# Performance work log

Measured on AMD Instinct MI355X. Metric: run time of the kernel, lower is better.

## Reference

```python
import jax, jax.numpy as jnp
import numpy as np

DIM = 384
NUM_HEADS = 12
WIN = (8, 8, 8)
Q_TOK = 1
K_TOK = 1
B = 64
N = WIN[0] * WIN[1] * WIN[2]  # 512


def _build_rel_index():
    t = max(Q_TOK, K_TOK)
    max_rel = [(w - 1) * t for w in WIN]
    nbins = [2 * m + 1 for m in max_rel]
    def coords(tok):
        axes = [np.arange(WIN[i]) * tok for i in range(3)]
        g = np.stack(np.meshgrid(*axes, indexing='ij'))  # [3, D, H, W]
        return g.reshape(3, -1)  # [3, N]
    cq = coords(Q_TOK)
    ck = coords(K_TOK)
    rel = (cq[:, :, None] - ck[:, None, :]).transpose(1, 2, 0)  # [N, N, 3]
    rel = rel + np.array(max_rel)
    idx = rel[..., 0] * (nbins[1] * nbins[2]) + rel[..., 1] * nbins[2] + rel[..., 2]
    return idx.astype(np.int32), nbins[0] * nbins[1] * nbins[2]


def setup_inputs() -> dict:
    key = jax.random.key(0)
    ks = jax.random.split(key, 7)
    rel_index_np, num_rel = _build_rel_index()
    s = 0.02
    return {
        'x1': jax.random.normal(ks[0], (B, N, DIM), jnp.float32),
        'x2': jax.random.normal(ks[1], (B, N, DIM), jnp.float32),
        'Wq': jax.random.normal(ks[2], (DIM, DIM), jnp.float32) * s,
        'Wkv': jax.random.normal(ks[3], (2 * DIM, DIM), jnp.float32) * s,
        'q_bias': jax.random.normal(ks[4], (DIM,), jnp.float32) * s,
        'v_bias': jax.random.normal(ks[5], (DIM,), jnp.float32) * s,
        'bias_table': jax.random.normal(ks[6], (num_rel, NUM_HEADS), jnp.float32) * s,
        'rel_index': jnp.asarray(rel_index_np),  # [N, N] int32
    }


def reference(x1, x2, Wq, Wkv, q_bias, v_bias, bias_table, rel_index):
    Bq, N1, C = x1.shape
    N2 = x2.shape[1]
    H = NUM_HEADS
    hd = C // H

    q = x1 @ Wq.T + q_bias                      # [B, N1, C]
    kv_bias = jnp.concatenate([jnp.zeros_like(v_bias), v_bias])
    kv = x2 @ Wkv.T + kv_bias                   # [B, N2, 2C]

    q = q.reshape(Bq, N1, H, hd).transpose(0, 2, 1, 3)   # [B, H, N1, hd]
    kv = kv.reshape(Bq, N2, 2, H, hd).transpose(2, 0, 3, 1, 4)
    k, v = kv[0], kv[1]                          # [B, H, N2, hd]

    # relative position bias: gather [N1, N2, H] -> [H, N1, N2]
    bias = bias_table[rel_index]                 # [N1, N2, H]
    bias = bias.transpose(2, 0, 1)               # [H, N1, N2]

    scale = 1.0 / jnp.sqrt(jnp.asarray(hd, q.dtype))
    scores = jnp.einsum('bhqd,bhkd->bhqk', q, k) * scale + bias[None]
    attn = jax.nn.softmax(scores, axis=-1)
    out = jnp.einsum('bhqk,bhkd->bhqd', attn, v)  # [B, H, N1, hd]
    return out.transpose(0, 2, 1, 3).reshape(Bq, N1, C)
```

## Files before the change

### kernel.cpp

```cpp
#include <hip/hip_runtime.h>

typedef unsigned short u16;
typedef unsigned int u32;
typedef __bf16 bf16x8 __attribute__((ext_vector_type(8)));
typedef float f32x4 __attribute__((ext_vector_type(4)));
typedef u16 u16x8 __attribute__((ext_vector_type(8)));
typedef u32 u32x4 __attribute__((ext_vector_type(4)));

#define NB 64
#define NN 512
#define NH 12
#define HD 32
#define DIM 384

static constexpr size_t QWS = (size_t)NB * NH * NN * HD;
#define LOG2E 1.4426950408889634f
#define QSCALE 0.25503486f

__device__ __forceinline__ u16 f2bf(float f) {
  __bf16 b = (__bf16)f;
  union { __bf16 b; u16 u; } v; v.b = b;
  return v.u;
}
__device__ __forceinline__ float lo16f(u32 w) {
  union { u32 u; float f; } v; v.u = w << 16;
  return v.f;
}
__device__ __forceinline__ float hi16f(u32 w) {
  union { u32 u; float f; } v; v.u = w & 0xffff0000u;
  return v.f;
}
__device__ __forceinline__ void gload16(const void* g, void* l) {
  __builtin_amdgcn_global_load_lds((const __attribute__((address_space(1))) u32*)g,
                                   (__attribute__((address_space(3))) u32*)l, 16, 0, 0);
}

__global__ __launch_bounds__(256) void prep_k(const float* __restrict__ table,
                                              const int* __restrict__ rel,
                                              const float* __restrict__ Wq,
                                              const float* __restrict__ Wkv,
                                              u32* __restrict__ beR,
                                              u16* __restrict__ Wf) {
  int bid = blockIdx.x;
  if (bid < 6144) {
    int t = bid * 256 + threadIdx.x;
    int word = t & 3;
    int lane = (t >> 2) & 63;
    int mf   = (t >> 8) & 3;
    int wv   = (t >> 10) & 7;
    int kt   = (t >> 13) & 15;
    int h    = t >> 17;
    int lr = lane & 15, lg = lane >> 4;
    int q = wv * 64 + mf * 16 + lr;
    int k = kt * 32 + (word >> 1) * 16 + lg * 4 + (word & 1) * 2;
    int i0 = rel[q * NN + k];
    int i1 = rel[q * NN + k + 1];
    u16 b0 = f2bf(table[i0 * NH + h] * LOG2E);
    u16 b1 = f2bf(table[i1 * NH + h] * LOG2E);
    beR[t] = (u32)b0 | ((u32)b1 << 16);
  } else {
    int t2 = (bid - 6144) * 256 + threadIdx.x;
    int lane = t2 & 63;
    int kk = (t2 >> 6) % 12;
    int cb = t2 / (12 * 64);
    int j = cb * 16 + (lane & 15);
    int k = kk * 32 + (lane >> 4) * 8;
    const float* wrow = (j < 384) ? (Wq + (size_t)j * DIM) : (Wkv + (size_t)(j - 384) * DIM);
    float4 a = *(const float4*)(wrow + k);
    float4 b = *(const float4*)(wrow + k + 4);
    u16x8 o = {f2bf(a.x), f2bf(a.y), f2bf(a.z), f2bf(a.w),
               f2bf(b.x), f2bf(b.y), f2bf(b.z), f2bf(b.w)};
    *(u16x8*)(Wf + (size_t)t2 * 8) = o;
  }
}

__global__ __launch_bounds__(512, 4) void qkv_proj_k(const float* __restrict__ x1,
                                                     const float* __restrict__ x2,
                                                     const float* __restrict__ qb,
                                                     const float* __restrict__ vb,
                                                     const u16* __restrict__ Wf,
                                                     u16* __restrict__ q_ws,
                                                     u16* __restrict__ k_ws,
                                                     u16* __restrict__ v_ws) {
  __shared__ __attribute__((aligned(16))) u16 Wbuf[2][12288];

  const int bid = blockIdx.x;
  const int is_q = bid >= 256;
  const int m0 = (bid & 255) * 128;
  const int tid = threadIdx.x, lane = tid & 63, w = tid >> 6;
  const int lg = lane >> 4, lr = lane & 15;
  const float* X = is_q ? x1 : x2;
  const int cb0 = is_q ? 0 : 24;
  const int nch = is_q ? 12 : 24;
  const char* wsrc = (const char*)(Wf + (size_t)cb0 * 12 * 64 * 8);
  const int bb = m0 >> 9;

  bf16x8 af[12];
  const float* xrow = X + (size_t)(m0 + w * 16 + lr) * DIM + lg * 8;
#pragma unroll
  for (int kk = 0; kk < 12; ++kk) {
    float4 a = *(const float4*)(xrow + kk * 32);
    float4 b = *(const float4*)(xrow + kk * 32 + 4);
    af[kk] = (bf16x8){(__bf16)a.x, (__bf16)a.y, (__bf16)a.z, (__bf16)a.w,
                      (__bf16)b.x, (__bf16)b.y, (__bf16)b.z, (__bf16)b.w};
  }

#pragma unroll
  for (int i = 0; i < 3; ++i) {
    int inst = w + i * 8;
    gload16(wsrc + inst * 1024 + lane * 16, (char*)&Wbuf[0][0] + inst * 1024 + lane * 16);
  }
  __syncthreads();

  for (int c = 0; c < nch; ++c) {
    if (c + 1 < nch) {
      const char* s = wsrc + (size_t)(c + 1) * 24576;
      char* d = (char*)&Wbuf[(c + 1) & 1][0];
#pragma unroll
      for (int i = 0; i < 3; ++i) {
        int inst = w + i * 8;
        gload16(s + inst * 1024 + lane * 16, d + inst * 1024 + lane * 16);
      }
    }
    const u16* wb = &Wbuf[c & 1][0];
#pragma unroll
    for (int lc = 0; lc < 2; ++lc) {
      f32x4 acc = {0.f, 0.f, 0.f, 0.f};
#pragma unroll
      for (int kk = 0; kk < 12; ++kk) {
        bf16x8 wf = *(const bf16x8*)(wb + ((lc * 12 + kk) * 64 + lane) * 8);
        acc = __builtin_amdgcn_mfma_f32_16x16x32_bf16(af[kk], wf, acc, 0, 0, 0);
      }
      int j = (cb0 + c * 2 + lc) * 16 + lr;
      int jj = is_q ? j : (j < 768 ? j - 384 : j - 768);
      float bv = is_q ? qb[jj] : (j >= 768 ? vb[jj] : 0.0f);
      float scale = is_q ? QSCALE : 1.0f;
      u16* dst = is_q ? q_ws : (j < 768 ? k_ws : v_ws);
      int hh = jj >> 5, dd = jj & 31;
      size_t basead = ((size_t)(bb * NH + hh) * NN) * HD + dd;
      int rowb = (m0 & 511) + w * 16 + lg * 4;
#pragma unroll
      for (int r = 0; r < 4; ++r)
        dst[basead + (size_t)(rowb + r) * HD] = f2bf((acc[r] + bv) * scale);
    }
    __syncthreads();
  }
}

__global__ __launch_bounds__(512, 4) void attn_k(const u16* __restrict__ qw,
                                                 const u16* __restrict__ kw,
                                                 const u16* __restrict__ vw,
                                                 const u32* __restrict__ beR,
                                                 float* __restrict__ out) {
  const int g = blockIdx.x;
  const int vv = (g & 7) * 96 + (g >> 3);
  const int h = vv >> 6, b = vv & 63;
  const size_t base = ((size_t)b * NH + h) * NN * HD;
  const u16* Q = qw + base;
  const u16* K = kw + base;
  const u16* V = vw + base;

  __shared__ u16 Ks[NN][40];
  __shared__ u16 Vtp[HD][520];

  const int tid = threadIdx.x;
  const int lane = tid & 63, w = tid >> 6;
  const int lg = lane >> 4, lr = lane & 15;
  const int q0 = w * 64;

  bf16x8 qf[4];
#pragma unroll
  for (int mf = 0; mf < 4; ++mf)
    qf[mf] = *(const bf16x8*)&Q[(q0 + mf * 16 + lr) * HD + lg * 8];

  for (int c = tid; c < 2048; c += 512) {
    int row = c >> 2, part = (c & 3) * 8;
    *(u16x8*)&Ks[row][part] = *(const u16x8*)&K[row * HD + part];
    u16x8 vld = *(const u16x8*)&V[row * HD + part];
    int kk = row & 31;
    int col = (row & ~31) + ((kk >> 2) & 3) * 8 + (kk >> 4) * 4 + (kk & 3);
#pragma unroll
    for (int j = 0; j < 8; ++j) Vtp[part + j][col] = vld[j];
  }
  __syncthreads();

  const u32* bstream = beR + ((((size_t)h * 16) * 8 + w) * 4) * 256 + lane * 4;

  f32x4 accOT[4][2] = {};
  float lsum[4] = {0.f, 0.f, 0.f, 0.f};

  for (int kt = 0; kt < 16; ++kt) {
    const int k0 = kt * 32;
    const u32* bkt = bstream + (size_t)kt * 8192;
    bf16x8 kf0 = *(const bf16x8*)&Ks[k0 + lr][lg * 8];
    bf16x8 kf1 = *(const bf16x8*)&Ks[k0 + 16 + lr][lg * 8];
    bf16x8 vp0 = *(const bf16x8*)&Vtp[lr][k0 + lg * 8];
    bf16x8 vp1 = *(const bf16x8*)&Vtp[16 + lr][k0 + lg * 8];
#pragma unroll
    for (int mf = 0; mf < 4; ++mf) {
      u32x4 bbv = *(const u32x4*)(bkt + mf * 256);
      f32x4 c0 = {lo16f(bbv.x), hi16f(bbv.x), lo16f(bbv.y), hi16f(bbv.y)};
      f32x4 c1 = {lo16f(bbv.z), hi16f(bbv.z), lo16f(bbv.w), hi16f(bbv.w)};
      f32x4 s0 = __builtin_amdgcn_mfma_f32_16x16x32_bf16(kf0, qf[mf], c0, 0, 0, 0);
      f32x4 s1 = __builtin_amdgcn_mfma_f32_16x16x32_bf16(kf1, qf[mf], c1, 0, 0, 0);
      float p0[4], p1[4];
#pragma unroll
      for (int r = 0; r < 4; ++r) {
        p0[r] = __builtin_amdgcn_exp2f(s0[r]);
        p1[r] = __builtin_amdgcn_exp2f(s1[r]);
      }
      lsum[mf] += ((p0[0] + p0[1]) + (p0[2] + p0[3])) +
                  ((p1[0] + p1[1]) + (p1[2] + p1[3]));
      bf16x8 pv = {(__bf16)p0[0], (__bf16)p0[1], (__bf16)p0[2], (__bf16)p0[3],
                   (__bf16)p1[0], (__bf16)p1[1], (__bf16)p1[2], (__bf16)p1[3]};
      accOT[mf][0] = __builtin_amdgcn_mfma_f32_16x16x32_bf16(vp0, pv, accOT[mf][0], 0, 0, 0);
      accOT[mf][1] = __builtin_amdgcn_mfma_f32_16x16x32_bf16(vp1, pv, accOT[mf][1], 0, 0, 0);
    }
  }

  float linv[4];
#pragma unroll
  for (int mf = 0; mf < 4; ++mf) {
    float s = lsum[mf];
    s += __shfl_xor(s, 16, 64);
    s += __shfl_xor(s, 32, 64);
    linv[mf] = 1.0f / s;
  }

  float* outp = out + ((size_t)b * NN) * DIM + h * HD;
#pragma unroll
  for (int mf = 0; mf < 4; ++mf) {
    int q = q0 + mf * 16 + lr;
#pragma unroll
    for (int nf = 0; nf < 2; ++nf) {
      float4 o = {accOT[mf][nf][0] * linv[mf], accOT[mf][nf][1] * linv[mf],
                  accOT[mf][nf][2] * linv[mf], accOT[mf][nf][3] * linv[mf]};
      *(float4*)&outp[(size_t)q * DIM + nf * 16 + lg * 4] = o;
    }
  }
}

extern "C" void kernel_launch(void* const* d_in, const int* in_sizes, int n_in,
                              void* d_out, int out_size, void* d_ws, size_t ws_size,
                              hipStream_t stream) {
  const float* x1    = (const float*)d_in[0];
  const float* x2    = (const float*)d_in[1];
  const float* Wq    = (const float*)d_in[2];
  const float* Wkv   = (const float*)d_in[3];
  const float* qb    = (const float*)d_in[4];
  const float* vb    = (const float*)d_in[5];
  const float* table = (const float*)d_in[6];
  const int*   rel   = (const int*)d_in[7];
  float* out = (float*)d_out;

  u16* ws   = (u16*)d_ws;
  u16* q_ws = ws;
  u16* k_ws = ws + QWS;
  u16* v_ws = ws + 2 * QWS;
  u32* beR  = (u32*)(ws + 3 * QWS);
  u16* Wf   = ws + 3 * QWS + 2 * 1572864;

  prep_k<<<6360, 256, 0, stream>>>(table, rel, Wq, Wkv, beR, Wf);
  qkv_proj_k<<<512, 512, 0, stream>>>(x1, x2, qb, vb, Wf, q_ws, k_ws, v_ws);
  attn_k<<<NB * NH, 512, 0, stream>>>(q_ws, k_ws, v_ws, beR, out);
}
```

Baseline: 107.1 us.

## Fuse bias-table gather into projection kernel and balance projection work per block

The weight conversion is split into its own small kernel, and the relative-position bias gather moves into the projection kernel as extra blocks. Projection blocks now each handle 12 chunks (Q, K, or V third) instead of Q blocks doing 12 and KV blocks doing 24, with a swizzled block order. This aims to overlap the memory-bound bias gather with the MFMA projection and remove the load imbalance between Q and KV blocks. The gather blocks carry the projection kernel's LDS and register footprint even though they do not use the shared buffer, which may limit how many run at once.

```diff
diff --git a/kernel.cpp b/kernel.cpp
--- a/kernel.cpp
+++ b/kernel.cpp
@@ -35,65 +35,68 @@
                                    (__attribute__((address_space(3))) u32*)l, 16, 0, 0);
 }
 
-__global__ __launch_bounds__(256) void prep_k(const float* __restrict__ table,
-                                              const int* __restrict__ rel,
-                                              const float* __restrict__ Wq,
-                                              const float* __restrict__ Wkv,
-                                              u32* __restrict__ beR,
-                                              u16* __restrict__ Wf) {
-  int bid = blockIdx.x;
-  if (bid < 6144) {
-    int t = bid * 256 + threadIdx.x;
+__global__ __launch_bounds__(256) void wprep_k(const float* __restrict__ Wq,
+                                               const float* __restrict__ Wkv,
+                                               u16* __restrict__ Wf) {
+  int t2 = blockIdx.x * 256 + threadIdx.x;
+  int lane = t2 & 63;
+  int kk = (t2 >> 6) % 12;
+  int cb = t2 / (12 * 64);
+  int j = cb * 16 + (lane & 15);
+  int k = kk * 32 + (lane >> 4) * 8;
+  const float* wrow = (j < 384) ? (Wq + (size_t)j * DIM) : (Wkv + (size_t)(j - 384) * DIM);
+  float4 a = *(const float4*)(wrow + k);
+  float4 b = *(const float4*)(wrow + k + 4);
+  u16x8 o = {f2bf(a.x), f2bf(a.y), f2bf(a.z), f2bf(a.w),
+             f2bf(b.x), f2bf(b.y), f2bf(b.z), f2bf(b.w)};
+  *(u16x8*)(Wf + (size_t)t2 * 8) = o;
+}
+
+__global__ __launch_bounds__(512, 4) void proj_bias_k(const float* __restrict__ x1,
+                                                      const float* __restrict__ x2,
+                                                      const float* __restrict__ qb,
+                                                      const float* __restrict__ vb,
+                                                      const u16* __restrict__ Wf,
+                                                      const float* __restrict__ table,
+                                                      const int* __restrict__ rel,
+                                                      u32* __restrict__ beR,
+                                                      u16* __restrict__ q_ws,
+                                                      u16* __restrict__ k_ws,
+                                                      u16* __restrict__ v_ws) {
+  __shared__ __attribute__((aligned(16))) u16 Wbuf[2][12288];
+
+  const int bid = blockIdx.x;
+  const int tid = threadIdx.x;
+
+  if (bid >= 768) {
+    int t = (bid - 768) * 512 + tid;
     int word = t & 3;
-    int lane = (t >> 2) & 63;
+    int lane2 = (t >> 2) & 63;
     int mf   = (t >> 8) & 3;
     int wv   = (t >> 10) & 7;
     int kt   = (t >> 13) & 15;
     int h    = t >> 17;
-    int lr = lane & 15, lg = lane >> 4;
-    int q = wv * 64 + mf * 16 + lr;
-    int k = kt * 32 + (word >> 1) * 16 + lg * 4 + (word & 1) * 2;
+    int lr2 = lane2 & 15, lg2 = lane2 >> 4;
+    int q = wv * 64 + mf * 16 + lr2;
+    int k = kt * 32 + (word >> 1) * 16 + lg2 * 4 + (word & 1) * 2;
     int i0 = rel[q * NN + k];
     int i1 = rel[q * NN + k + 1];
     u16 b0 = f2bf(table[i0 * NH + h] * LOG2E);
     u16 b1 = f2bf(table[i1 * NH + h] * LOG2E);
     beR[t] = (u32)b0 | ((u32)b1 << 16);
-  } else {
-    int t2 = (bid - 6144) * 256 + threadIdx.x;
-    int lane = t2 & 63;
-    int kk = (t2 >> 6) % 12;
-    int cb = t2 / (12 * 64);
-    int j = cb * 16 + (lane & 15);
-    int k = kk * 32 + (lane >> 4) * 8;
-    const float* wrow = (j < 384) ? (Wq + (size_t)j * DIM) : (Wkv + (size_t)(j - 384) * DIM);
-    float4 a = *(const float4*)(wrow + k);
-    float4 b = *(const float4*)(wrow + k + 4);
-    u16x8 o = {f2bf(a.x), f2bf(a.y), f2bf(a.z), f2bf(a.w),
-               f2bf(b.x), f2bf(b.y), f2bf(b.z), f2bf(b.w)};
-    *(u16x8*)(Wf + (size_t)t2 * 8) = o;
-  }
-}
-
-__global__ __launch_bounds__(512, 4) void qkv_proj_k(const float* __restrict__ x1,
-                                                     const float* __restrict__ x2,
-                                                     const float* __restrict__ qb,
-                                                     const float* __restrict__ vb,
-                                                     const u16* __restrict__ Wf,
-                                                     u16* __restrict__ q_ws,
-                                                     u16* __restrict__ k_ws,
-                                                     u16* __restrict__ v_ws) {
-  __shared__ __attribute__((aligned(16))) u16 Wbuf[2][12288];
-
-  const int bid = blockIdx.x;
-  const int is_q = bid >= 256;
-  const int m0 = (bid & 255) * 128;
-  const int tid = threadIdx.x, lane = tid & 63, w = tid >> 6;
+    return;
+  }
+
+  const int vv = (bid & 7) * 96 + (bid >> 3);
+  const int t3 = vv >> 8;
+  const int m0 = (vv & 255) * 128;
+  const int cb0 = t3 * 24;
+  const int lane = tid & 63, w = tid >> 6;
   const int lg = lane >> 4, lr = lane & 15;
-  const float* X = is_q ? x1 : x2;
-  const int cb0 = is_q ? 0 : 24;
-  const int nch = is_q ? 12 : 24;
-  const char* wsrc = (const char*)(Wf + (size_t)cb0 * 12 * 64 * 8);
-  const int bb = m0 >> 9;
+  const float* X = (t3 == 0) ? x1 : x2;
+  const int is_q = (t3 == 0);
+  const char* wsrc = (const char*)(Wf + (size_t)cb0 * 6144);
+  const int bb = m0 >> 9, m0r = m0 & 511;
 
   bf16x8 af[12];
   const float* xrow = X + (size_t)(m0 + w * 16 + lr) * DIM + lg * 8;
@@ -112,8 +115,11 @@
   }
   __syncthreads();
 
-  for (int c = 0; c < nch; ++c) {
-    if (c + 1 < nch) {
+  const float scale = is_q ? QSCALE : 1.0f;
+  const int rowb = m0r + w * 16 + lg * 4;
+
+  for (int c = 0; c < 12; ++c) {
+    if (c + 1 < 12) {
       const char* s = wsrc + (size_t)(c + 1) * 24576;
       char* d = (char*)&Wbuf[(c + 1) & 1][0];
 #pragma unroll
@@ -134,14 +140,12 @@
       int j = (cb0 + c * 2 + lc) * 16 + lr;
       int jj = is_q ? j : (j < 768 ? j - 384 : j - 768);
       float bv = is_q ? qb[jj] : (j >= 768 ? vb[jj] : 0.0f);
-      float scale = is_q ? QSCALE : 1.0f;
-      u16* dst = is_q ? q_ws : (j < 768 ? k_ws : v_ws);
+      u16* dstp = is_q ? q_ws : (j < 768 ? k_ws : v_ws);
       int hh = jj >> 5, dd = jj & 31;
       size_t basead = ((size_t)(bb * NH + hh) * NN) * HD + dd;
-      int rowb = (m0 & 511) + w * 16 + lg * 4;
 #pragma unroll
       for (int r = 0; r < 4; ++r)
-        dst[basead + (size_t)(rowb + r) * HD] = f2bf((acc[r] + bv) * scale);
+        dstp[basead + (size_t)(rowb + r) * HD] = f2bf((acc[r] + bv) * scale);
     }
     __syncthreads();
   }
@@ -260,7 +264,8 @@
   u32* beR  = (u32*)(ws + 3 * QWS);
   u16* Wf   = ws + 3 * QWS + 2 * 1572864;
 
-  prep_k<<<6360, 256, 0, stream>>>(table, rel, Wq, Wkv, beR, Wf);
-  qkv_proj_k<<<512, 512, 0, stream>>>(x1, x2, qb, vb, Wf, q_ws, k_ws, v_ws);
+  wprep_k<<<216, 256, 0, stream>>>(Wq, Wkv, Wf);
+  proj_bias_k<<<3840, 512, 0, stream>>>(x1, x2, qb, vb, Wf, table, rel, beR,
+                                        q_ws, k_ws, v_ws);
   attn_k<<<NB * NH, 512, 0, stream>>>(q_ws, k_ws, v_ws, beR, out);
 }
```

Result: slower. 118.0 us (+10.1%).

## Fuse QKV projection into attention kernel per batch-head block

Applied to the files above, without the earlier changes.

Removes the separate QKV projection kernel and computes each head's Q, K and V projections inside the attention block, writing them straight into shared memory. This eliminates the bf16 q/k/v workspace write and reread and one kernel launch. In exchange, every head block rereads and reconverts the full fp32 x1/x2 rows of its batch, so input traffic rises about twelvefold, and the launch bound is relaxed to two blocks per CU.

```diff
diff --git a/kernel.cpp b/kernel.cpp
--- a/kernel.cpp
+++ b/kernel.cpp
@@ -4,6 +4,7 @@
 typedef unsigned int u32;
 typedef __bf16 bf16x8 __attribute__((ext_vector_type(8)));
 typedef float f32x4 __attribute__((ext_vector_type(4)));
+typedef u16 u16x4 __attribute__((ext_vector_type(4)));
 typedef u16 u16x8 __attribute__((ext_vector_type(8)));
 typedef u32 u32x4 __attribute__((ext_vector_type(4)));
 
@@ -13,7 +14,6 @@
 #define HD 32
 #define DIM 384
 
-static constexpr size_t QWS = (size_t)NB * NH * NN * HD;
 #define LOG2E 1.4426950408889634f
 #define QSCALE 0.25503486f
 
@@ -29,10 +29,6 @@
 __device__ __forceinline__ float hi16f(u32 w) {
   union { u32 u; float f; } v; v.u = w & 0xffff0000u;
   return v.f;
-}
-__device__ __forceinline__ void gload16(const void* g, void* l) {
-  __builtin_amdgcn_global_load_lds((const __attribute__((address_space(1))) u32*)g,
-                                   (__attribute__((address_space(3))) u32*)l, 16, 0, 0);
 }
 
 __global__ __launch_bounds__(256) void prep_k(const float* __restrict__ table,
@@ -74,91 +70,16 @@
   }
 }
 
-__global__ __launch_bounds__(512, 4) void qkv_proj_k(const float* __restrict__ x1,
-                                                     const float* __restrict__ x2,
-                                                     const float* __restrict__ qb,
-                                                     const float* __restrict__ vb,
-                                                     const u16* __restrict__ Wf,
-                                                     u16* __restrict__ q_ws,
-                                                     u16* __restrict__ k_ws,
-                                                     u16* __restrict__ v_ws) {
-  __shared__ __attribute__((aligned(16))) u16 Wbuf[2][12288];
-
-  const int bid = blockIdx.x;
-  const int is_q = bid >= 256;
-  const int m0 = (bid & 255) * 128;
-  const int tid = threadIdx.x, lane = tid & 63, w = tid >> 6;
-  const int lg = lane >> 4, lr = lane & 15;
-  const float* X = is_q ? x1 : x2;
-  const int cb0 = is_q ? 0 : 24;
-  const int nch = is_q ? 12 : 24;
-  const char* wsrc = (const char*)(Wf + (size_t)cb0 * 12 * 64 * 8);
-  const int bb = m0 >> 9;
-
-  bf16x8 af[12];
-  const float* xrow = X + (size_t)(m0 + w * 16 + lr) * DIM + lg * 8;
-#pragma unroll
-  for (int kk = 0; kk < 12; ++kk) {
-    float4 a = *(const float4*)(xrow + kk * 32);
-    float4 b = *(const float4*)(xrow + kk * 32 + 4);
-    af[kk] = (bf16x8){(__bf16)a.x, (__bf16)a.y, (__bf16)a.z, (__bf16)a.w,
-                      (__bf16)b.x, (__bf16)b.y, (__bf16)b.z, (__bf16)b.w};
-  }
-
-#pragma unroll
-  for (int i = 0; i < 3; ++i) {
-    int inst = w + i * 8;
-    gload16(wsrc + inst * 1024 + lane * 16, (char*)&Wbuf[0][0] + inst * 1024 + lane * 16);
-  }
-  __syncthreads();
-
-  for (int c = 0; c < nch; ++c) {
-    if (c + 1 < nch) {
-      const char* s = wsrc + (size_t)(c + 1) * 24576;
-      char* d = (char*)&Wbuf[(c + 1) & 1][0];
-#pragma unroll
-      for (int i = 0; i < 3; ++i) {
-        int inst = w + i * 8;
-        gload16(s + inst * 1024 + lane * 16, d + inst * 1024 + lane * 16);
-      }
-    }
-    const u16* wb = &Wbuf[c & 1][0];
-#pragma unroll
-    for (int lc = 0; lc < 2; ++lc) {
-      f32x4 acc = {0.f, 0.f, 0.f, 0.f};
-#pragma unroll
-      for (int kk = 0; kk < 12; ++kk) {
-        bf16x8 wf = *(const bf16x8*)(wb + ((lc * 12 + kk) * 64 + lane) * 8);
-        acc = __builtin_amdgcn_mfma_f32_16x16x32_bf16(af[kk], wf, acc, 0, 0, 0);
-      }
-      int j = (cb0 + c * 2 + lc) * 16 + lr;
-      int jj = is_q ? j : (j < 768 ? j - 384 : j - 768);
-      float bv = is_q ? qb[jj] : (j >= 768 ? vb[jj] : 0.0f);
-      float scale = is_q ? QSCALE : 1.0f;
-      u16* dst = is_q ? q_ws : (j < 768 ? k_ws : v_ws);
-      int hh = jj >> 5, dd = jj & 31;
-      size_t basead = ((size_t)(bb * NH + hh) * NN) * HD + dd;
-      int rowb = (m0 & 511) + w * 16 + lg * 4;
-#pragma unroll
-      for (int r = 0; r < 4; ++r)
-        dst[basead + (size_t)(rowb + r) * HD] = f2bf((acc[r] + bv) * scale);
-    }
-    __syncthreads();
-  }
-}
-
-__global__ __launch_bounds__(512, 4) void attn_k(const u16* __restrict__ qw,
-                                                 const u16* __restrict__ kw,
-                                                 const u16* __restrict__ vw,
-                                                 const u32* __restrict__ beR,
-                                                 float* __restrict__ out) {
+__global__ __launch_bounds__(512, 2) void fused_k(const float* __restrict__ x1,
+                                                  const float* __restrict__ x2,
+                                                  const float* __restrict__ qb,
+                                                  const float* __restrict__ vb,
+                                                  const u16* __restrict__ Wf,
+                                                  const u32* __restrict__ beR,
+                                                  float* __restrict__ out) {
   const int g = blockIdx.x;
   const int vv = (g & 7) * 96 + (g >> 3);
-  const int h = vv >> 6, b = vv & 63;
-  const size_t base = ((size_t)b * NH + h) * NN * HD;
-  const u16* Q = qw + base;
-  const u16* K = kw + base;
-  const u16* V = vw + base;
+  const int b = vv / 12, h = vv % 12;
 
   __shared__ u16 Ks[NN][40];
   __shared__ u16 Vtp[HD][520];
@@ -168,19 +89,91 @@
   const int lg = lane >> 4, lr = lane & 15;
   const int q0 = w * 64;
 
+  const float* x1w = x1 + ((size_t)b * NN + q0 + lr) * DIM + lg * 8;
+  const u16* wfQ = Wf + ((size_t)(2 * h) * 12 * 64 + lane) * 8;
+  f32x4 aq[4][2] = {};
+#pragma unroll
+  for (int kk = 0; kk < 12; ++kk) {
+    bf16x8 af[4];
+#pragma unroll
+    for (int mf = 0; mf < 4; ++mf) {
+      const float* p = x1w + (size_t)mf * 16 * DIM + kk * 32;
+      float4 a = *(const float4*)p;
+      float4 c = *(const float4*)(p + 4);
+      af[mf] = (bf16x8){(__bf16)a.x, (__bf16)a.y, (__bf16)a.z, (__bf16)a.w,
+                        (__bf16)c.x, (__bf16)c.y, (__bf16)c.z, (__bf16)c.w};
+    }
+    bf16x8 wq0 = *(const bf16x8*)(wfQ + (size_t)kk * 512);
+    bf16x8 wq1 = *(const bf16x8*)(wfQ + (size_t)(12 + kk) * 512);
+#pragma unroll
+    for (int mf = 0; mf < 4; ++mf) {
+      aq[mf][0] = __builtin_amdgcn_mfma_f32_16x16x32_bf16(wq0, af[mf], aq[mf][0], 0, 0, 0);
+      aq[mf][1] = __builtin_amdgcn_mfma_f32_16x16x32_bf16(wq1, af[mf], aq[mf][1], 0, 0, 0);
+    }
+  }
+#pragma unroll
+  for (int nf = 0; nf < 2; ++nf) {
+    float4 qbv = *(const float4*)(qb + h * 32 + nf * 16 + lg * 4);
+#pragma unroll
+    for (int mf = 0; mf < 4; ++mf) {
+      u16x4 o = {f2bf((aq[mf][nf][0] + qbv.x) * QSCALE),
+                 f2bf((aq[mf][nf][1] + qbv.y) * QSCALE),
+                 f2bf((aq[mf][nf][2] + qbv.z) * QSCALE),
+                 f2bf((aq[mf][nf][3] + qbv.w) * QSCALE)};
+      *(u16x4*)&Ks[q0 + mf * 16 + lr][nf * 16 + lg * 4] = o;
+    }
+  }
   bf16x8 qf[4];
 #pragma unroll
   for (int mf = 0; mf < 4; ++mf)
-    qf[mf] = *(const bf16x8*)&Q[(q0 + mf * 16 + lr) * HD + lg * 8];
-
-  for (int c = tid; c < 2048; c += 512) {
-    int row = c >> 2, part = (c & 3) * 8;
-    *(u16x8*)&Ks[row][part] = *(const u16x8*)&K[row * HD + part];
-    u16x8 vld = *(const u16x8*)&V[row * HD + part];
-    int kk = row & 31;
-    int col = (row & ~31) + ((kk >> 2) & 3) * 8 + (kk >> 4) * 4 + (kk & 3);
-#pragma unroll
-    for (int j = 0; j < 8; ++j) Vtp[part + j][col] = vld[j];
+    qf[mf] = *(const bf16x8*)&Ks[q0 + mf * 16 + lr][lg * 8];
+
+  const float* x2w = x2 + ((size_t)b * NN + q0 + lr) * DIM + lg * 8;
+  const u16* wfK = Wf + ((size_t)(24 + 2 * h) * 12 * 64 + lane) * 8;
+  const u16* wfV = Wf + ((size_t)(48 + 2 * h) * 12 * 64 + lane) * 8;
+  f32x4 ak[4][2] = {}, av[4][2] = {};
+#pragma unroll
+  for (int kk = 0; kk < 12; ++kk) {
+    bf16x8 af[4];
+#pragma unroll
+    for (int mf = 0; mf < 4; ++mf) {
+      const float* p = x2w + (size_t)mf * 16 * DIM + kk * 32;
+      float4 a = *(const float4*)p;
+      float4 c = *(const float4*)(p + 4);
+      af[mf] = (bf16x8){(__bf16)a.x, (__bf16)a.y, (__bf16)a.z, (__bf16)a.w,
+                        (__bf16)c.x, (__bf16)c.y, (__bf16)c.z, (__bf16)c.w};
+    }
+    bf16x8 wk0 = *(const bf16x8*)(wfK + (size_t)kk * 512);
+    bf16x8 wk1 = *(const bf16x8*)(wfK + (size_t)(12 + kk) * 512);
+    bf16x8 wv0 = *(const bf16x8*)(wfV + (size_t)kk * 512);
+    bf16x8 wv1 = *(const bf16x8*)(wfV + (size_t)(12 + kk) * 512);
+#pragma unroll
+    for (int mf = 0; mf < 4; ++mf) {
+      ak[mf][0] = __builtin_amdgcn_mfma_f32_16x16x32_bf16(wk0, af[mf], ak[mf][0], 0, 0, 0);
+      ak[mf][1] = __builtin_amdgcn_mfma_f32_16x16x32_bf16(wk1, af[mf], ak[mf][1], 0, 0, 0);
+      av[mf][0] = __builtin_amdgcn_mfma_f32_16x16x32_bf16(af[mf], wv0, av[mf][0], 0, 0, 0);
+      av[mf][1] = __builtin_amdgcn_mfma_f32_16x16x32_bf16(af[mf], wv1, av[mf][1], 0, 0, 0);
+    }
+  }
+#pragma unroll
+  for (int mf = 0; mf < 4; ++mf)
+#pragma unroll
+    for (int nf = 0; nf < 2; ++nf) {
+      u16x4 o = {f2bf(ak[mf][nf][0]), f2bf(ak[mf][nf][1]),
+                 f2bf(ak[mf][nf][2]), f2bf(ak[mf][nf][3])};
+      *(u16x4*)&Ks[q0 + mf * 16 + lr][nf * 16 + lg * 4] = o;
+    }
+#pragma unroll
+  for (int mf = 0; mf < 4; ++mf) {
+    int colb = q0 + (mf >> 1) * 32 + 8 * lg + 4 * (mf & 1);
+#pragma unroll
+    for (int nf = 0; nf < 2; ++nf) {
+      int d = nf * 16 + lr;
+      float bv = vb[h * 32 + d];
+      u16x4 o = {f2bf(av[mf][nf][0] + bv), f2bf(av[mf][nf][1] + bv),
+                 f2bf(av[mf][nf][2] + bv), f2bf(av[mf][nf][3] + bv)};
+      *(u16x4*)&Vtp[d][colb] = o;
+    }
   }
   __syncthreads();
 
@@ -253,14 +246,9 @@
   const int*   rel   = (const int*)d_in[7];
   float* out = (float*)d_out;
 
-  u16* ws   = (u16*)d_ws;
-  u16* q_ws = ws;
-  u16* k_ws = ws + QWS;
-  u16* v_ws = ws + 2 * QWS;
-  u32* beR  = (u32*)(ws + 3 * QWS);
-  u16* Wf   = ws + 3 * QWS + 2 * 1572864;
+  u32* beR = (u32*)d_ws;
+  u16* Wf  = (u16*)(beR + 1572864);
 
   prep_k<<<6360, 256, 0, stream>>>(table, rel, Wq, Wkv, beR, Wf);
-  qkv_proj_k<<<512, 512, 0, stream>>>(x1, x2, qb, vb, Wf, q_ws, k_ws, v_ws);
-  attn_k<<<NB * NH, 512, 0, stream>>>(q_ws, k_ws, v_ws, beR, out);
-}
+  fused_k<<<NB * NH, 512, 0, stream>>>(x1, x2, qb, vb, Wf, beR, out);
+}
```

After: 210.5 us. 96.5% more time.
